# Performance work log

Hardware: AMD Instinct MI355X
Metric: run time of the kernel (lower is better)

The kernel has to match this reference:

```python
import jax, jax.numpy as jnp
import numpy as np

H = 1024  # latent_dim / GRU hidden size


def setup_inputs() -> dict:
    key = jax.random.key(0)
    ks = jax.random.split(key, 7)
    B, T, E, V = 16, 256, 512, 32000
    return {
        "latent_samples": jax.random.normal(ks[0], (B, H), jnp.float32),
        "true_outputs": jax.random.normal(ks[1], (B, T, E), jnp.float32),
        "gru_kernel": jax.random.normal(ks[2], (E, 3 * H), jnp.float32) * 0.02,
        "gru_rec_kernel": jax.random.normal(ks[3], (H, 3 * H), jnp.float32) * 0.02,
        "gru_bias": jax.random.normal(ks[4], (2, 3 * H), jnp.float32) * 0.02,
        "dense_w": jax.random.normal(ks[5], (H, V), jnp.float32) * 0.02,
        "dense_b": jax.random.normal(ks[6], (V,), jnp.float32) * 0.02,
    }


def reference(latent_samples, true_outputs, gru_kernel, gru_rec_kernel, gru_bias, dense_w, dense_b):
    # teacher_forcing_decode: GRU over true_outputs[:, :-1, :] with initial state latent_samples,
    # then TimeDistributed Dense to vocab logits. Keras GRU, reset_after=True, gate order z|r|h.
    teacher = true_outputs[:, :-1, :]                      # [B, T-1, E]
    # Precompute all input projections at once: [B, T-1, 3H]
    x_proj = jnp.einsum('bte,eg->btg', teacher, gru_kernel) + gru_bias[0]
    rec_bias = gru_bias[1]

    def step(h, x_t):  # h: [B,H], x_t: [B,3H]
        rec = h @ gru_rec_kernel + rec_bias              # [B,3H]
        xz, xr, xh = jnp.split(x_t, 3, axis=-1)
        rz, rr, rh = jnp.split(rec, 3, axis=-1)
        z = jax.nn.sigmoid(xz + rz)
        r = jax.nn.sigmoid(xr + rr)
        hh = jnp.tanh(xh + r * rh)
        h_new = z * h + (1.0 - z) * hh
        return h_new, h_new

    _, hs = jax.lax.scan(step, latent_samples, jnp.swapaxes(x_proj, 0, 1))  # hs: [T-1, B, H]
    gru_out = jnp.swapaxes(hs, 0, 1)                       # [B, T-1, H]
    logits = jnp.einsum('bth,hv->btv', gru_out, dense_w) + dense_b
    return logits
```

## Files before the change

kernel.cpp:

```cpp
#include <hip/hip_runtime.h>


typedef __attribute__((ext_vector_type(8))) short s16x8;
typedef __attribute__((ext_vector_type(4))) float f32x4;
typedef __attribute__((ext_vector_type(4))) int   i32x4;

#define B_      16
#define TSTEPS  255
#define H_      1024
#define G_      3072
#define E_      512
#define V_      32000
#define MROWS   4080
#define MPAD    4096
#define NBLK_SCAN 64
#define NWORK     448
#define NBLK_TOT  512
#define NTILE_RB  32
#define NTILE_CB  250
#define FSTRIDE   16

__device__ __forceinline__ short f2bf(float f) {
  unsigned u = __float_as_uint(f);
  u = (u + 0x7fffu + ((u >> 16) & 1u)) >> 16;
  return (short)u;
}

__device__ __forceinline__ float frcp(float x) {
  float r;
  asm("v_rcp_f32 %0, %1" : "=v"(r) : "v"(x));
  return r;
}

#define GLD_C(dst, p)                                                          \
  asm volatile("global_load_dwordx4 %0, %1, off"                               \
               : "=v"(dst) : "v"(p) : "memory")

__device__ __forceinline__ void gload_lds16(const short* g, void* l) {
  __builtin_amdgcn_global_load_lds((const __attribute__((address_space(1))) void*)g,
                                   (__attribute__((address_space(3))) void*)l,
                                   16, 0, 0);
}


__global__ void transpose_cvt(const float* __restrict__ src, short* __restrict__ dst,
                              int K, int N) {
  __shared__ float tile[32][33];
  const int n0 = blockIdx.x * 32, k0 = blockIdx.y * 32;
  const int tx = threadIdx.x, ty0 = threadIdx.y;
#pragma unroll
  for (int yy = 0; yy < 4; ++yy) {
    int ty = ty0 + yy * 8;
    tile[ty][tx] = src[(size_t)(k0 + ty) * N + (n0 + tx)];
  }
  __syncthreads();
#pragma unroll
  for (int yy = 0; yy < 4; ++yy) {
    int ty = ty0 + yy * 8;
    dst[(size_t)(n0 + ty) * K + (k0 + tx)] = f2bf(tile[tx][ty]);
  }
}

__global__ void pack_teacher(const float* __restrict__ src, short* __restrict__ dst) {
  int idx = blockIdx.x * 256 + threadIdx.x;
  int row = idx >> 6;
  int c8 = (idx & 63) << 3;
  int t = row >> 4, b = row & 15;
  s16x8 v = {};
  if (t < TSTEPS) {
    const float* s = src + ((size_t)(b * 256 + t)) * E_ + c8;
#pragma unroll
    for (int j = 0; j < 8; ++j) v[j] = f2bf(s[j]);
  }
  *(s16x8*)(dst + (size_t)row * E_ + c8) = v;
}

__global__ void init_h(const float* __restrict__ latent, short* __restrict__ hist) {
  int i = blockIdx.x * 256 + threadIdx.x;
  hist[i] = f2bf(latent[i]);
}

__global__ __launch_bounds__(256) void gemm_bf16(
    const short* __restrict__ A, const short* __restrict__ BT,
    const float* __restrict__ bias, float* __restrict__ C, int N, int K) {
  const int tid = threadIdx.x;
  const int lane = tid & 63, w = tid >> 6;
  const int r = lane & 15, q = lane >> 4;
  const int bm = blockIdx.y * 128, bn = blockIdx.x * 128;
  const int wm = bm + (w >> 1) * 64, wn = bn + (w & 1) * 64;
  const short* Ab = A + (size_t)(wm + r) * K + q * 8;
  const short* Bb = BT + (size_t)(wn + r) * K + q * 8;
  f32x4 acc[4][4] = {};
  s16x8 a0[4], b0[4], a1[4], b1[4];
  const int nk = K >> 5;
#define GL(AA, BB, kk)                                                         \
  {                                                                            \
    _Pragma("unroll") for (int i = 0; i < 4; ++i) {                            \
      AA[i] = *(const s16x8*)(Ab + (size_t)i * 16 * K + (kk) * 32);            \
    }                                                                          \
    _Pragma("unroll") for (int j = 0; j < 4; ++j) {                            \
      BB[j] = *(const s16x8*)(Bb + (size_t)j * 16 * K + (kk) * 32);            \
    }                                                                          \
  }
#define MM(AA, BB)                                                             \
  {                                                                            \
    _Pragma("unroll") for (int i = 0; i < 4; ++i)                              \
        _Pragma("unroll") for (int j = 0; j < 4; ++j)                          \
            acc[i][j] = __builtin_amdgcn_mfma_f32_16x16x32_bf16(               \
                AA[i], BB[j], acc[i][j], 0, 0, 0);                             \
  }
  GL(a0, b0, 0)
#pragma unroll 1
  for (int ks = 0; ks < nk; ks += 2) {
    GL(a1, b1, ks + 1)
    MM(a0, b0)
    if (ks + 2 < nk) GL(a0, b0, ks + 2)
    MM(a1, b1)
  }
#undef GL
#undef MM
#pragma unroll
  for (int j = 0; j < 4; ++j) {
    const int col = wn + j * 16 + r;
    const float bv = bias[col];
#pragma unroll
    for (int i = 0; i < 4; ++i) {
#pragma unroll
      for (int rr = 0; rr < 4; ++rr) {
        const int row = wm + i * 16 + q * 4 + rr;
        C[(size_t)row * N + col] = acc[i][j][rr] + bv;
      }
    }
  }
}

__global__ __launch_bounds__(256, 2) void fused_scan_gemm(
    const short* __restrict__ WrecT,
    const float* __restrict__ xproj,
    const float* __restrict__ bias1,
    const float* __restrict__ latent,
    short* __restrict__ hist,
    const short* __restrict__ DwT,
    const float* __restrict__ db,
    float* __restrict__ out,
    unsigned* __restrict__ sync) {
  const int tid = threadIdx.x, lane = tid & 63, w = tid >> 6;
  const int r = lane & 15, q = lane >> 4;
  __shared__ s16x8 smem_v[2048];
  unsigned* scanflag = sync;
  unsigned* frontier = sync + 1024;

  if (blockIdx.x < NBLK_SCAN) {
    __builtin_amdgcn_s_setprio(3);
    float (*red)[3][64][4] = (float(*)[3][64][4])smem_v;
    const int c = blockIdx.x;
    s16x8 wb[3][8];
#pragma unroll
    for (int g = 0; g < 3; ++g)
#pragma unroll
      for (int s = 0; s < 8; ++s)
        wb[g][s] = *(const s16x8*)(WrecT + (size_t)(g * 1024 + c * 16 + r) * 1024 +
                                   (w * 8 + s) * 32 + q * 8);

    const int m = tid >> 4, nl = tid & 15, col = c * 16 + nl;
    float h = latent[m * 1024 + col];
    const float bz = bias1[col], brr = bias1[1024 + col], bhh = bias1[2048 + col];
    const float* xb = xproj + (size_t)m * G_;
    float xz = xb[col], xr = xb[1024 + col], xh = xb[2048 + col];

    for (int t = 0; t < TSTEPS; ++t) {
      const short* hrow = hist + ((size_t)t * 16 + r) * 1024 + w * 256 + q * 8;
      i32x4 afi[8];
#pragma unroll
      for (int s = 0; s < 8; ++s) GLD_C(afi[s], hrow + s * 32);
      asm volatile("s_waitcnt vmcnt(0)"
                   : "+v"(afi[0]), "+v"(afi[1]), "+v"(afi[2]), "+v"(afi[3]),
                     "+v"(afi[4]), "+v"(afi[5]), "+v"(afi[6]), "+v"(afi[7])
                   :: "memory");
      __builtin_amdgcn_sched_barrier(0);
      f32x4 acc[3] = {};
#pragma unroll
      for (int s = 0; s < 8; ++s) {
        const s16x8 af = *(const s16x8*)&afi[s];
        acc[0] = __builtin_amdgcn_mfma_f32_16x16x32_bf16(af, wb[0][s], acc[0], 0, 0, 0);
        acc[1] = __builtin_amdgcn_mfma_f32_16x16x32_bf16(af, wb[1][s], acc[1], 0, 0, 0);
        acc[2] = __builtin_amdgcn_mfma_f32_16x16x32_bf16(af, wb[2][s], acc[2], 0, 0, 0);
      }
      *(f32x4*)&red[w][0][lane][0] = acc[0];
      *(f32x4*)&red[w][1][lane][0] = acc[1];
      *(f32x4*)&red[w][2][lane][0] = acc[2];
      __syncthreads();
      const int rl = (m >> 2) * 16 + nl, ri = m & 3;
      float rz = bz, rr2 = brr, rh = bhh;
#pragma unroll
      for (int ww = 0; ww < 4; ++ww) {
        rz += red[ww][0][rl][ri];
        rr2 += red[ww][1][rl][ri];
        rh += red[ww][2][rl][ri];
      }
      const float z = frcp(1.f + __expf(-(xz + rz)));
      const float rg = frcp(1.f + __expf(-(xr + rr2)));
      const float hh = tanhf(xh + rg * rh);
      h = z * h + (1.f - z) * hh;
      const unsigned hb16 = (unsigned short)f2bf(h);
      const unsigned nb = __shfl(hb16, lane | 1, 64);
      const unsigned pv = hb16 | (nb << 16);
      if (!(tid & 1))
        __hip_atomic_store(
            (unsigned*)hist + (((size_t)(t + 1) * 16 + m) * 1024 + col) / 2,
            pv, __ATOMIC_RELAXED, __HIP_MEMORY_SCOPE_AGENT);
      __syncthreads();
      if (tid == 0)
        __hip_atomic_store(&scanflag[c * FSTRIDE], (unsigned)(t + 1),
                           __ATOMIC_RELAXED, __HIP_MEMORY_SCOPE_AGENT);
      if ((t & 7) == 7) {
        if (tid == 0)
          __hip_atomic_store(&frontier[c * FSTRIDE], (unsigned)(t + 1),
                             __ATOMIC_RELAXED, __HIP_MEMORY_SCOPE_AGENT);
      }
      {
        const float* xn = xb + (size_t)(t + 1) * 16 * G_;
        xz = xn[col]; xr = xn[1024 + col]; xh = xn[2048 + col];
      }
      if (t < TSTEPS - 1) {
        const unsigned* fp = &scanflag[lane * FSTRIDE];
        unsigned v = __hip_atomic_load(fp, __ATOMIC_RELAXED,
                                       __HIP_MEMORY_SCOPE_AGENT);
        while (!__all(v > (unsigned)t))
          v = __hip_atomic_load(fp, __ATOMIC_RELAXED, __HIP_MEMORY_SCOPE_AGENT);
      }
    }
    if (tid == 0)
      __hip_atomic_store(&frontier[c * FSTRIDE], 256u,
                         __ATOMIC_RELAXED, __HIP_MEMORY_SCOPE_AGENT);
  } else {
    char* sb = (char*)smem_v;
    const int wr = w >> 1, wc = w & 1;
    const int xterm = ((q ^ ((r >> 1) & 3)) << 4);
    const int swz8 = (((lane & 3) ^ ((lane >> 3) & 3)) << 3);
    const int j = blockIdx.x - NBLK_SCAN;
#pragma unroll 1
    for (int tq = j; tq < NTILE_RB * NTILE_CB; tq += NWORK) {
      const int rb = tq / NTILE_CB, cb = tq - rb * NTILE_CB;
      const unsigned need = (unsigned)(rb < 31 ? 8 * rb + 8 : 256);
      unsigned v = __hip_atomic_load(&frontier[lane * FSTRIDE], __ATOMIC_RELAXED,
                                     __HIP_MEMORY_SCOPE_AGENT);
      while (!__all(v >= need)) {
        __builtin_amdgcn_s_sleep(32);
        v = __hip_atomic_load(&frontier[lane * FSTRIDE], __ATOMIC_RELAXED,
                              __HIP_MEMORY_SCOPE_AGENT);
      }
      const short* Ag = hist + (size_t)16 * 1024 + (size_t)rb * 128 * 1024;
      const short* Bg = DwT + (size_t)cb * 128 * 1024;
      f32x4 acc[4][4] = {};
#define STAGE(buf, kk)                                                         \
  {                                                                            \
    _Pragma("unroll") for (int it = 0; it < 2; ++it) {                         \
      const size_t go = (size_t)(w * 32 + it * 16 + (lane >> 2)) * 1024 +      \
                        (kk) * 32 + swz8;                                      \
      char* lb2 = sb + (buf) * 16384 + w * 2048 + it * 1024;                   \
      gload_lds16(Ag + go, lb2);                                               \
      gload_lds16(Bg + go, lb2 + 8192);                                        \
    }                                                                          \
  }
      STAGE(0, 0)
#pragma unroll 1
      for (int kk = 0; kk < 32; ++kk) {
        __syncthreads();
        if (kk < 31) STAGE((kk + 1) & 1, kk + 1)
        const char* ab = sb + (kk & 1) * 16384;
        s16x8 af[4], bf[4];
#pragma unroll
        for (int i = 0; i < 4; ++i)
          af[i] = *(const s16x8*)(ab + (wr * 64 + i * 16 + r) * 64 + xterm);
#pragma unroll
        for (int j5 = 0; j5 < 4; ++j5)
          bf[j5] = *(const s16x8*)(ab + 8192 + (wc * 64 + j5 * 16 + r) * 64 + xterm);
#pragma unroll
        for (int i = 0; i < 4; ++i)
#pragma unroll
          for (int j5 = 0; j5 < 4; ++j5)
            acc[i][j5] = __builtin_amdgcn_mfma_f32_16x16x32_bf16(
                af[i], bf[j5], acc[i][j5], 0, 0, 0);
      }
#undef STAGE
      const int wm = rb * 128 + wr * 64, wn = cb * 128 + wc * 64;
#pragma unroll
      for (int j2 = 0; j2 < 4; ++j2) {
        const int col = wn + j2 * 16 + r;
        const float bv = db[col];
#pragma unroll
        for (int i = 0; i < 4; ++i) {
#pragma unroll
          for (int rr = 0; rr < 4; ++rr) {
            const int arow = wm + i * 16 + q * 4 + rr;
            const int t = arow >> 4, mm = arow & 15;
            if (t < TSTEPS)
              __builtin_nontemporal_store(
                  acc[i][j2][rr] + bv,
                  &out[(size_t)(mm * TSTEPS + t) * V_ + col]);
          }
        }
      }
      __syncthreads();
    }
  }
}

extern "C" void kernel_launch(void* const* d_in, const int* in_sizes, int n_in,
                              void* d_out, int out_size, void* d_ws, size_t ws_size,
                              hipStream_t stream) {
  const float* latent = (const float*)d_in[0];
  const float* trueo  = (const float*)d_in[1];
  const float* gk     = (const float*)d_in[2];
  const float* grk    = (const float*)d_in[3];
  const float* gbias  = (const float*)d_in[4];
  const float* dw     = (const float*)d_in[5];
  const float* db     = (const float*)d_in[6];
  float* out = (float*)d_out;
  char* ws = (char*)d_ws;
  short*    WrecT  = (short*)(ws + 0);
  short*    GkT    = (short*)(ws + 6291456);
  short*    DwT    = (short*)(ws + 9437184);
  short*    teachA = (short*)(ws + 74973184);
  float*    xproj  = (float*)(ws + 79167488);
  short*    hist   = (short*)(ws + 129499136);
  unsigned* syncb  = (unsigned*)(ws + 137920512);

  hipMemsetAsync(syncb, 0, 8192, stream);
  transpose_cvt<<<dim3(96, 32), dim3(32, 8), 0, stream>>>(grk, WrecT, 1024, 3072);
  transpose_cvt<<<dim3(96, 16), dim3(32, 8), 0, stream>>>(gk, GkT, 512, 3072);
  transpose_cvt<<<dim3(1000, 32), dim3(32, 8), 0, stream>>>(dw, DwT, 1024, 32000);
  pack_teacher<<<1024, 256, 0, stream>>>(trueo, teachA);
  gemm_bf16<<<dim3(24, 32), 256, 0, stream>>>(teachA, GkT, gbias, xproj, G_, E_);
  init_h<<<64, 256, 0, stream>>>(latent, hist);
  fused_scan_gemm<<<NBLK_TOT, 256, 0, stream>>>(WrecT, xproj, gbias + G_, latent,
                                                hist, DwT, db, out, syncb);
}
```

Baseline: 923.8 us.

## Fuse dense weight transpose-convert into worker blocks to overlap with scan

Removes the standalone transpose_cvt launch for the large dense weight and has the first 250 GEMM worker blocks convert their 128-column slab to bf16 while the recurrent scan runs, publishing per-column-block ready flags that GEMM tiles poll before reading. It also replaces tanhf with an exp/rcp formulation and moves the next-step xproj loads ahead of the barrier in the scan loop. The aim is to hide the weight conversion behind the serial scan, at the cost of extra flag polling and write-through stores whose visibility relies on relaxed atomics.

```diff
diff --git a/kernel.cpp b/kernel.cpp
--- a/kernel.cpp
+++ b/kernel.cpp
@@ -11,8 +11,6 @@
 #define G_      3072
 #define E_      512
 #define V_      32000
-#define MROWS   4080
-#define MPAD    4096
 #define NBLK_SCAN 64
 #define NWORK     448
 #define NBLK_TOT  512
@@ -35,6 +33,8 @@
 #define GLD_C(dst, p)                                                          \
   asm volatile("global_load_dwordx4 %0, %1, off"                               \
                : "=v"(dst) : "v"(p) : "memory")
+#define ST32_WT(p, x)                                                          \
+  asm volatile("global_store_dword %0, %1, off sc0 sc1" :: "v"(p), "v"(x) : "memory")
 
 __device__ __forceinline__ void gload_lds16(const short* g, void* l) {
   __builtin_amdgcn_global_load_lds((const __attribute__((address_space(1))) void*)g,
@@ -140,7 +140,8 @@
     const float* __restrict__ bias1,
     const float* __restrict__ latent,
     short* __restrict__ hist,
-    const short* __restrict__ DwT,
+    short* __restrict__ DwT,
+    const float* __restrict__ dw,
     const float* __restrict__ db,
     float* __restrict__ out,
     unsigned* __restrict__ sync) {
@@ -149,6 +150,7 @@
   __shared__ s16x8 smem_v[2048];
   unsigned* scanflag = sync;
   unsigned* frontier = sync + 1024;
+  unsigned* cbflag   = sync + 2048;
 
   if (blockIdx.x < NBLK_SCAN) {
     __builtin_amdgcn_s_setprio(3);
@@ -200,7 +202,8 @@
       }
       const float z = frcp(1.f + __expf(-(xz + rz)));
       const float rg = frcp(1.f + __expf(-(xr + rr2)));
-      const float hh = tanhf(xh + rg * rh);
+      const float e2 = __expf(2.f * (xh + rg * rh));
+      const float hh = 1.f - 2.f * frcp(e2 + 1.f);
       h = z * h + (1.f - z) * hh;
       const unsigned hb16 = (unsigned short)f2bf(h);
       const unsigned nb = __shfl(hb16, lane | 1, 64);
@@ -209,18 +212,17 @@
         __hip_atomic_store(
             (unsigned*)hist + (((size_t)(t + 1) * 16 + m) * 1024 + col) / 2,
             pv, __ATOMIC_RELAXED, __HIP_MEMORY_SCOPE_AGENT);
-      __syncthreads();
-      if (tid == 0)
-        __hip_atomic_store(&scanflag[c * FSTRIDE], (unsigned)(t + 1),
-                           __ATOMIC_RELAXED, __HIP_MEMORY_SCOPE_AGENT);
-      if ((t & 7) == 7) {
-        if (tid == 0)
-          __hip_atomic_store(&frontier[c * FSTRIDE], (unsigned)(t + 1),
-                             __ATOMIC_RELAXED, __HIP_MEMORY_SCOPE_AGENT);
-      }
       {
         const float* xn = xb + (size_t)(t + 1) * 16 * G_;
         xz = xn[col]; xr = xn[1024 + col]; xh = xn[2048 + col];
+      }
+      __syncthreads();
+      if (tid == 0) {
+        __hip_atomic_store(&scanflag[c * FSTRIDE], (unsigned)(t + 1),
+                           __ATOMIC_RELAXED, __HIP_MEMORY_SCOPE_AGENT);
+        if ((t & 7) == 7)
+          __hip_atomic_store(&frontier[c * FSTRIDE], (unsigned)(t + 1),
+                             __ATOMIC_RELAXED, __HIP_MEMORY_SCOPE_AGENT);
       }
       if (t < TSTEPS - 1) {
         const unsigned* fp = &scanflag[lane * FSTRIDE];
@@ -239,6 +241,37 @@
     const int xterm = ((q ^ ((r >> 1) & 3)) << 4);
     const int swz8 = (((lane & 3) ^ ((lane >> 3) & 3)) << 3);
     const int j = blockIdx.x - NBLK_SCAN;
+
+    if (j < NTILE_CB) {
+      float (*tl)[33] = (float(*)[33])sb;
+      const int tx = tid & 31, ty0 = tid >> 5;
+      const int wy = tid >> 4, wx = tid & 15;
+#pragma unroll 1
+      for (int it = 0; it < 128; ++it) {
+        const int n0 = j * 128 + (it >> 5) * 32, k0 = (it & 31) * 32;
+        __syncthreads();
+#pragma unroll
+        for (int yy = 0; yy < 4; ++yy) {
+          int ty = ty0 + yy * 8;
+          tl[ty][tx] = dw[(size_t)(k0 + ty) * V_ + (n0 + tx)];
+        }
+        __syncthreads();
+#pragma unroll
+        for (int yy = 0; yy < 2; ++yy) {
+          int ty = wy + yy * 16;
+          unsigned pv = (unsigned)(unsigned short)f2bf(tl[2 * wx][ty]) |
+                        ((unsigned)(unsigned short)f2bf(tl[2 * wx + 1][ty]) << 16);
+          unsigned* dst = (unsigned*)DwT + ((size_t)(n0 + ty) * 1024 + k0) / 2 + wx;
+          ST32_WT(dst, pv);
+        }
+      }
+      asm volatile("s_waitcnt vmcnt(0)" ::: "memory");
+      __syncthreads();
+      if (tid == 0)
+        __hip_atomic_store(&cbflag[j * FSTRIDE], 1u,
+                           __ATOMIC_RELAXED, __HIP_MEMORY_SCOPE_AGENT);
+    }
+
 #pragma unroll 1
     for (int tq = j; tq < NTILE_RB * NTILE_CB; tq += NWORK) {
       const int rb = tq / NTILE_CB, cb = tq - rb * NTILE_CB;
@@ -249,6 +282,15 @@
         __builtin_amdgcn_s_sleep(32);
         v = __hip_atomic_load(&frontier[lane * FSTRIDE], __ATOMIC_RELAXED,
                               __HIP_MEMORY_SCOPE_AGENT);
+      }
+      {
+        unsigned cv = __hip_atomic_load(&cbflag[cb * FSTRIDE], __ATOMIC_RELAXED,
+                                        __HIP_MEMORY_SCOPE_AGENT);
+        while (!cv) {
+          __builtin_amdgcn_s_sleep(16);
+          cv = __hip_atomic_load(&cbflag[cb * FSTRIDE], __ATOMIC_RELAXED,
+                                 __HIP_MEMORY_SCOPE_AGENT);
+        }
       }
       const short* Ag = hist + (size_t)16 * 1024 + (size_t)rb * 128 * 1024;
       const short* Bg = DwT + (size_t)cb * 128 * 1024;
@@ -327,13 +369,12 @@
   short*    hist   = (short*)(ws + 129499136);
   unsigned* syncb  = (unsigned*)(ws + 137920512);
 
-  hipMemsetAsync(syncb, 0, 8192, stream);
+  hipMemsetAsync(syncb, 0, 24576, stream);
   transpose_cvt<<<dim3(96, 32), dim3(32, 8), 0, stream>>>(grk, WrecT, 1024, 3072);
   transpose_cvt<<<dim3(96, 16), dim3(32, 8), 0, stream>>>(gk, GkT, 512, 3072);
-  transpose_cvt<<<dim3(1000, 32), dim3(32, 8), 0, stream>>>(dw, DwT, 1024, 32000);
   pack_teacher<<<1024, 256, 0, stream>>>(trueo, teachA);
   gemm_bf16<<<dim3(24, 32), 256, 0, stream>>>(teachA, GkT, gbias, xproj, G_, E_);
   init_h<<<64, 256, 0, stream>>>(latent, hist);
   fused_scan_gemm<<<NBLK_TOT, 256, 0, stream>>>(WrecT, xproj, gbias + G_, latent,
-                                                hist, DwT, db, out, syncb);
-}
+                                                hist, DwT, dw, db, out, syncb);
+}
```

Result: slower. 988.2 us (+7.0%).

## Stage scan state in LDS, publish with write-through stores, rebalance worker blocks

Applied to the files above, without the earlier changes.

Each scan block now gathers its new hidden-state slice into LDS and publishes it with one wave of 128-bit write-through stores, then the step flag, instead of per-thread 32-bit atomics. The reduction buffer is double-buffered by step parity. tanh is replaced by an exp/rcp formula. Blocks 256–319 now exit immediately, leaving 384 GEMM workers, apparently to keep the scan blocks from sharing CUs with GEMM blocks. The goal is a shorter critical path per recurrent step, at the cost of less GEMM parallelism and a less accurate tanh that can overflow for large inputs.

```diff
diff --git a/kernel.cpp b/kernel.cpp
--- a/kernel.cpp
+++ b/kernel.cpp
@@ -11,10 +11,8 @@
 #define G_      3072
 #define E_      512
 #define V_      32000
-#define MROWS   4080
-#define MPAD    4096
 #define NBLK_SCAN 64
-#define NWORK     448
+#define NWORK     384
 #define NBLK_TOT  512
 #define NTILE_RB  32
 #define NTILE_CB  250
@@ -35,6 +33,10 @@
 #define GLD_C(dst, p)                                                          \
   asm volatile("global_load_dwordx4 %0, %1, off"                               \
                : "=v"(dst) : "v"(p) : "memory")
+#define ST32_WT(p, x)                                                          \
+  asm volatile("global_store_dword %0, %1, off sc0 sc1" :: "v"(p), "v"(x) : "memory")
+#define ST128_WT(p, x)                                                         \
+  asm volatile("global_store_dwordx4 %0, %1, off sc0 sc1" :: "v"(p), "v"(x) : "memory")
 
 __device__ __forceinline__ void gload_lds16(const short* g, void* l) {
   __builtin_amdgcn_global_load_lds((const __attribute__((address_space(1))) void*)g,
@@ -149,11 +151,15 @@
   __shared__ s16x8 smem_v[2048];
   unsigned* scanflag = sync;
   unsigned* frontier = sync + 1024;
-
-  if (blockIdx.x < NBLK_SCAN) {
+  const int bid = blockIdx.x;
+
+  if (bid >= 256 && bid < 320) return;
+
+  if (bid < NBLK_SCAN) {
     __builtin_amdgcn_s_setprio(3);
-    float (*red)[3][64][4] = (float(*)[3][64][4])smem_v;
-    const int c = blockIdx.x;
+    float (*red)[4][3][64][4] = (float(*)[4][3][64][4])smem_v;
+    unsigned short* hsl = (unsigned short*)((char*)smem_v + 24576);
+    const int c = bid;
     s16x8 wb[3][8];
 #pragma unroll
     for (int g = 0; g < 3; ++g)
@@ -186,37 +192,39 @@
         acc[1] = __builtin_amdgcn_mfma_f32_16x16x32_bf16(af, wb[1][s], acc[1], 0, 0, 0);
         acc[2] = __builtin_amdgcn_mfma_f32_16x16x32_bf16(af, wb[2][s], acc[2], 0, 0, 0);
       }
-      *(f32x4*)&red[w][0][lane][0] = acc[0];
-      *(f32x4*)&red[w][1][lane][0] = acc[1];
-      *(f32x4*)&red[w][2][lane][0] = acc[2];
+      *(f32x4*)&red[t & 1][w][0][lane][0] = acc[0];
+      *(f32x4*)&red[t & 1][w][1][lane][0] = acc[1];
+      *(f32x4*)&red[t & 1][w][2][lane][0] = acc[2];
       __syncthreads();
       const int rl = (m >> 2) * 16 + nl, ri = m & 3;
       float rz = bz, rr2 = brr, rh = bhh;
 #pragma unroll
       for (int ww = 0; ww < 4; ++ww) {
-        rz += red[ww][0][rl][ri];
-        rr2 += red[ww][1][rl][ri];
-        rh += red[ww][2][rl][ri];
+        rz += red[t & 1][ww][0][rl][ri];
+        rr2 += red[t & 1][ww][1][rl][ri];
+        rh += red[t & 1][ww][2][rl][ri];
       }
       const float z = frcp(1.f + __expf(-(xz + rz)));
       const float rg = frcp(1.f + __expf(-(xr + rr2)));
-      const float hh = tanhf(xh + rg * rh);
+      const float e2 = __expf(2.f * (xh + rg * rh));
+      const float hh = 1.f - 2.f * frcp(e2 + 1.f);
       h = z * h + (1.f - z) * hh;
-      const unsigned hb16 = (unsigned short)f2bf(h);
-      const unsigned nb = __shfl(hb16, lane | 1, 64);
-      const unsigned pv = hb16 | (nb << 16);
-      if (!(tid & 1))
-        __hip_atomic_store(
-            (unsigned*)hist + (((size_t)(t + 1) * 16 + m) * 1024 + col) / 2,
-            pv, __ATOMIC_RELAXED, __HIP_MEMORY_SCOPE_AGENT);
+      hsl[(t & 1) * 256 + m * 16 + nl] = (unsigned short)f2bf(h);
       __syncthreads();
-      if (tid == 0)
-        __hip_atomic_store(&scanflag[c * FSTRIDE], (unsigned)(t + 1),
-                           __ATOMIC_RELAXED, __HIP_MEMORY_SCOPE_AGENT);
-      if ((t & 7) == 7) {
-        if (tid == 0)
-          __hip_atomic_store(&frontier[c * FSTRIDE], (unsigned)(t + 1),
-                             __ATOMIC_RELAXED, __HIP_MEMORY_SCOPE_AGENT);
+      if (w == 0) {
+        if (lane < 32) {
+          const i32x4 hv =
+              *(const i32x4*)((const char*)(hsl + (t & 1) * 256) + lane * 16);
+          unsigned* dst = (unsigned*)(hist +
+              ((size_t)(t + 1) * 16 + (lane >> 1)) * 1024 + c * 16 + (lane & 1) * 8);
+          ST128_WT(dst, hv);
+          asm volatile("s_waitcnt vmcnt(0)" ::: "memory");
+          if (lane == 0) {
+            if (t < TSTEPS - 1) ST32_WT(&scanflag[c * FSTRIDE], (unsigned)(t + 1));
+            if ((t & 7) == 7) ST32_WT(&frontier[c * FSTRIDE], (unsigned)(t + 1));
+            if (t == TSTEPS - 1) ST32_WT(&frontier[c * FSTRIDE], 256u);
+          }
+        }
       }
       {
         const float* xn = xb + (size_t)(t + 1) * 16 * G_;
@@ -230,15 +238,12 @@
           v = __hip_atomic_load(fp, __ATOMIC_RELAXED, __HIP_MEMORY_SCOPE_AGENT);
       }
     }
-    if (tid == 0)
-      __hip_atomic_store(&frontier[c * FSTRIDE], 256u,
-                         __ATOMIC_RELAXED, __HIP_MEMORY_SCOPE_AGENT);
   } else {
     char* sb = (char*)smem_v;
     const int wr = w >> 1, wc = w & 1;
     const int xterm = ((q ^ ((r >> 1) & 3)) << 4);
     const int swz8 = (((lane & 3) ^ ((lane >> 3) & 3)) << 3);
-    const int j = blockIdx.x - NBLK_SCAN;
+    const int j = (bid < 256) ? (bid - NBLK_SCAN) : (bid - 128);
 #pragma unroll 1
     for (int tq = j; tq < NTILE_RB * NTILE_CB; tq += NWORK) {
       const int rb = tq / NTILE_CB, cb = tq - rb * NTILE_CB;
```

Measured after the change: 962.5 us. +4.2%, slower.

## Pack scan flags into bytes, prefetch next xproj, and use a cheaper tanh

Applied to the files above, without the earlier changes.

The per-block step flags and frontier counters shrink from 16-word-strided unsigned slots to packed single bytes. They are written and polled with cache-bypassing sc0 sc1 byte stores and loads, so one 64-byte line serves all scan blocks and a poll touches one line instead of many. The next timestep's input projection loads are issued together with the h-history loads and only waited on after the barrier, hiding their latency behind the MFMA step. tanhf is replaced with an exp/rcp formula, which costs a little accuracy and relies on the hand-written memory ordering of the new flag accesses.

```diff
diff --git a/kernel.cpp b/kernel.cpp
--- a/kernel.cpp
+++ b/kernel.cpp
@@ -11,14 +11,11 @@
 #define G_      3072
 #define E_      512
 #define V_      32000
-#define MROWS   4080
-#define MPAD    4096
 #define NBLK_SCAN 64
 #define NWORK     448
 #define NBLK_TOT  512
 #define NTILE_RB  32
 #define NTILE_CB  250
-#define FSTRIDE   16
 
 __device__ __forceinline__ short f2bf(float f) {
   unsigned u = __float_as_uint(f);
@@ -35,6 +32,13 @@
 #define GLD_C(dst, p)                                                          \
   asm volatile("global_load_dwordx4 %0, %1, off"                               \
                : "=v"(dst) : "v"(p) : "memory")
+#define LDF32(v, p)                                                            \
+  asm volatile("global_load_dword %0, %1, off" : "=v"(v) : "v"(p))
+#define ST8_WT(p, x)                                                           \
+  asm volatile("global_store_byte %0, %1, off sc0 sc1" :: "v"(p), "v"(x) : "memory")
+#define LD8_SC(v, p)                                                           \
+  asm volatile("global_load_ubyte %0, %1, off sc0 sc1\n\ts_waitcnt vmcnt(0)"   \
+               : "=v"(v) : "v"(p) : "memory")
 
 __device__ __forceinline__ void gload_lds16(const short* g, void* l) {
   __builtin_amdgcn_global_load_lds((const __attribute__((address_space(1))) void*)g,
@@ -143,12 +147,12 @@
     const short* __restrict__ DwT,
     const float* __restrict__ db,
     float* __restrict__ out,
-    unsigned* __restrict__ sync) {
+    unsigned char* __restrict__ sync) {
   const int tid = threadIdx.x, lane = tid & 63, w = tid >> 6;
   const int r = lane & 15, q = lane >> 4;
   __shared__ s16x8 smem_v[2048];
-  unsigned* scanflag = sync;
-  unsigned* frontier = sync + 1024;
+  unsigned char* scanB  = sync;
+  unsigned char* frontB = sync + 64;
 
   if (blockIdx.x < NBLK_SCAN) {
     __builtin_amdgcn_s_setprio(3);
@@ -173,7 +177,12 @@
       i32x4 afi[8];
 #pragma unroll
       for (int s = 0; s < 8; ++s) GLD_C(afi[s], hrow + s * 32);
-      asm volatile("s_waitcnt vmcnt(0)"
+      float nz, nr, nh;
+      {
+        const float* xn = xb + (size_t)(t + 1) * 16 * G_;
+        LDF32(nz, xn + col); LDF32(nr, xn + 1024 + col); LDF32(nh, xn + 2048 + col);
+      }
+      asm volatile("s_waitcnt vmcnt(3)"
                    : "+v"(afi[0]), "+v"(afi[1]), "+v"(afi[2]), "+v"(afi[3]),
                      "+v"(afi[4]), "+v"(afi[5]), "+v"(afi[6]), "+v"(afi[7])
                    :: "memory");
@@ -200,7 +209,8 @@
       }
       const float z = frcp(1.f + __expf(-(xz + rz)));
       const float rg = frcp(1.f + __expf(-(xr + rr2)));
-      const float hh = tanhf(xh + rg * rh);
+      const float e2 = __expf(2.f * (xh + rg * rh));
+      const float hh = 1.f - 2.f * frcp(e2 + 1.f);
       h = z * h + (1.f - z) * hh;
       const unsigned hb16 = (unsigned short)f2bf(h);
       const unsigned nb = __shfl(hb16, lane | 1, 64);
@@ -210,29 +220,21 @@
             (unsigned*)hist + (((size_t)(t + 1) * 16 + m) * 1024 + col) / 2,
             pv, __ATOMIC_RELAXED, __HIP_MEMORY_SCOPE_AGENT);
       __syncthreads();
-      if (tid == 0)
-        __hip_atomic_store(&scanflag[c * FSTRIDE], (unsigned)(t + 1),
-                           __ATOMIC_RELAXED, __HIP_MEMORY_SCOPE_AGENT);
-      if ((t & 7) == 7) {
-        if (tid == 0)
-          __hip_atomic_store(&frontier[c * FSTRIDE], (unsigned)(t + 1),
-                             __ATOMIC_RELAXED, __HIP_MEMORY_SCOPE_AGENT);
-      }
-      {
-        const float* xn = xb + (size_t)(t + 1) * 16 * G_;
-        xz = xn[col]; xr = xn[1024 + col]; xh = xn[2048 + col];
+      asm volatile("s_waitcnt vmcnt(0)"
+                   : "+v"(nz), "+v"(nr), "+v"(nh) :: "memory");
+      __builtin_amdgcn_sched_barrier(0);
+      xz = nz; xr = nr; xh = nh;
+      if (tid == 0) {
+        ST8_WT(scanB + c, (unsigned)(t + 1));
+        if ((t & 7) == 7) ST8_WT(frontB + c, (unsigned)((t + 1) >> 3));
+        if (t == TSTEPS - 1) ST8_WT(frontB + c, 32u);
       }
       if (t < TSTEPS - 1) {
-        const unsigned* fp = &scanflag[lane * FSTRIDE];
-        unsigned v = __hip_atomic_load(fp, __ATOMIC_RELAXED,
-                                       __HIP_MEMORY_SCOPE_AGENT);
-        while (!__all(v > (unsigned)t))
-          v = __hip_atomic_load(fp, __ATOMIC_RELAXED, __HIP_MEMORY_SCOPE_AGENT);
+        unsigned v;
+        LD8_SC(v, scanB + lane);
+        while (!__all(v > (unsigned)t)) LD8_SC(v, scanB + lane);
       }
     }
-    if (tid == 0)
-      __hip_atomic_store(&frontier[c * FSTRIDE], 256u,
-                         __ATOMIC_RELAXED, __HIP_MEMORY_SCOPE_AGENT);
   } else {
     char* sb = (char*)smem_v;
     const int wr = w >> 1, wc = w & 1;
@@ -242,13 +244,12 @@
 #pragma unroll 1
     for (int tq = j; tq < NTILE_RB * NTILE_CB; tq += NWORK) {
       const int rb = tq / NTILE_CB, cb = tq - rb * NTILE_CB;
-      const unsigned need = (unsigned)(rb < 31 ? 8 * rb + 8 : 256);
-      unsigned v = __hip_atomic_load(&frontier[lane * FSTRIDE], __ATOMIC_RELAXED,
-                                     __HIP_MEMORY_SCOPE_AGENT);
+      const unsigned need = (unsigned)(rb < 31 ? rb + 1 : 32);
+      unsigned v;
+      LD8_SC(v, frontB + lane);
       while (!__all(v >= need)) {
         __builtin_amdgcn_s_sleep(32);
-        v = __hip_atomic_load(&frontier[lane * FSTRIDE], __ATOMIC_RELAXED,
-                              __HIP_MEMORY_SCOPE_AGENT);
+        LD8_SC(v, frontB + lane);
       }
       const short* Ag = hist + (size_t)16 * 1024 + (size_t)rb * 128 * 1024;
       const short* Bg = DwT + (size_t)cb * 128 * 1024;
@@ -325,9 +326,9 @@
   short*    teachA = (short*)(ws + 74973184);
   float*    xproj  = (float*)(ws + 79167488);
   short*    hist   = (short*)(ws + 129499136);
-  unsigned* syncb  = (unsigned*)(ws + 137920512);
-
-  hipMemsetAsync(syncb, 0, 8192, stream);
+  unsigned char* syncb = (unsigned char*)(ws + 137920512);
+
+  hipMemsetAsync(syncb, 0, 256, stream);
   transpose_cvt<<<dim3(96, 32), dim3(32, 8), 0, stream>>>(grk, WrecT, 1024, 3072);
   transpose_cvt<<<dim3(96, 16), dim3(32, 8), 0, stream>>>(gk, GkT, 512, 3072);
   transpose_cvt<<<dim3(1000, 32), dim3(32, 8), 0, stream>>>(dw, DwT, 1024, 32000);
@@ -335,5 +336,5 @@
   gemm_bf16<<<dim3(24, 32), 256, 0, stream>>>(teachA, GkT, gbias, xproj, G_, E_);
   init_h<<<64, 256, 0, stream>>>(latent, hist);
   fused_scan_gemm<<<NBLK_TOT, 256, 0, stream>>>(WrecT, xproj, gbias + G_, latent,
-                                                hist, DwT, db, out, syncb);
-}
+                                                hist, DwT, db, out, (unsigned char*)syncb);
+}
```

Measured after the change: 2.421 ms. 2.62x slower.
